# Performance work log

Measured on AMD Instinct MI355X. Metric: run time of the kernel, lower is better.

## Reference

```python
import jax, jax.numpy as jnp
import numpy as np

# Mamba2 defaults: d_model=256, d_state=64, d_conv=4, expand=2, headdim=64, ngroups=1
D_MODEL = 256
NB = 2            # num_blocks
D_STATE = 64
D_CONV = 4
D_INNER = 2 * D_MODEL          # 512
HEADDIM = 64
NHEADS = D_INNER // HEADDIM    # 8
CONV_DIM = D_INNER + 2 * D_STATE           # 640
D_IN_PROJ = 2 * D_INNER + 2 * D_STATE + NHEADS  # 1160
EPS = 1e-5


def setup_inputs() -> dict:
    key = jax.random.key(0)
    ks = jax.random.split(key, 10)
    x = jax.random.normal(ks[0], (8, 32, 32, D_MODEL), dtype=jnp.float32)
    in_proj_w = jax.random.normal(ks[1], (NB, D_IN_PROJ, D_MODEL), dtype=jnp.float32) * 0.02
    conv_w = jax.random.normal(ks[2], (NB, CONV_DIM, 1, D_CONV), dtype=jnp.float32) * 0.2
    conv_b = jax.random.normal(ks[3], (NB, CONV_DIM), dtype=jnp.float32) * 0.02
    dt_bias = jax.random.normal(ks[4], (NB, NHEADS), dtype=jnp.float32) * 0.5
    # A_log = log(A), A ~ U[1,16) as in mamba2 init
    A_log = jnp.log(jax.random.uniform(ks[5], (NB, NHEADS), minval=1.0, maxval=16.0, dtype=jnp.float32))
    D = jax.random.normal(ks[6], (NB, NHEADS), dtype=jnp.float32) * 0.1 + 1.0
    norm_w = jnp.ones((NB, D_INNER), dtype=jnp.float32)
    out_proj_w = jax.random.normal(ks[7], (NB, D_MODEL, D_INNER), dtype=jnp.float32) * 0.02
    return {"x": x, "in_proj_w": in_proj_w, "conv_w": conv_w, "conv_b": conv_b,
            "dt_bias": dt_bias, "A_log": A_log, "D": D, "norm_w": norm_w,
            "out_proj_w": out_proj_w}


def _mamba2_block(h, wi, cw, cb, dtb, a_log, d_skip, nw, wo):
    B, L, _ = h.shape
    zxbcdt = jnp.einsum('blc,pc->blp', h, wi)                 # (B,L,1160)
    z = zxbcdt[..., :D_INNER]                                 # (B,L,512)
    xBC = zxbcdt[..., D_INNER:D_INNER + CONV_DIM]             # (B,L,640)
    dt = jax.nn.softplus(zxbcdt[..., -NHEADS:] + dtb)         # (B,L,8)

    # causal depthwise conv1d, kernel 4, left pad 3
    xBC = jax.lax.conv_general_dilated(
        xBC.swapaxes(1, 2), cw, window_strides=(1,), padding=[(D_CONV - 1, 0)],
        dimension_numbers=('NCH', 'OIH', 'NCH'), feature_group_count=CONV_DIM)
    xBC = jax.nn.silu((xBC + cb[None, :, None]).swapaxes(1, 2))  # (B,L,640)

    xs = xBC[..., :D_INNER].reshape(B, L, NHEADS, HEADDIM)    # (B,L,h,p)
    Bm = xBC[..., D_INNER:D_INNER + D_STATE]                  # (B,L,s) ngroups=1
    Cm = xBC[..., D_INNER + D_STATE:]                         # (B,L,s)

    A = -jnp.exp(a_log)                                       # (h,)
    dA = jnp.exp(dt * A)                                      # (B,L,h)

    def step(s, inp):
        dA_t, dt_t, x_t, B_t, C_t = inp  # (B,h),(B,h),(B,h,p),(B,s),(B,s)
        s = s * dA_t[:, :, None, None] + (dt_t[:, :, None] * x_t)[..., None] * B_t[:, None, None, :]
        y = jnp.einsum('bhps,bs->bhp', s, C_t)
        return s, y

    s0 = jnp.zeros((B, NHEADS, HEADDIM, D_STATE), dtype=h.dtype)
    _, ys = jax.lax.scan(step, s0, (dA.swapaxes(0, 1), dt.swapaxes(0, 1),
                                    xs.swapaxes(0, 1), Bm.swapaxes(0, 1), Cm.swapaxes(0, 1)))
    y = ys.swapaxes(0, 1) + d_skip[:, None] * xs              # (B,L,h,p)
    y = y.reshape(B, L, D_INNER) * jax.nn.silu(z)             # gate
    y = y * jax.lax.rsqrt(jnp.mean(y * y, axis=-1, keepdims=True) + EPS) * nw  # gated RMSNorm
    return jnp.einsum('bld,cd->blc', y, wo)


def reference(x, in_proj_w, conv_w, conv_b, dt_bias, A_log, D, norm_w, out_proj_w):
    B, H, W, C = x.shape
    h = x.reshape(B, H * W, C)
    for i in range(NB):  # stacked blocks; Dropout is identity at inference
        h = _mamba2_block(h, in_proj_w[i], conv_w[i], conv_b[i], dt_bias[i],
                          A_log[i], D[i], norm_w[i], out_proj_w[i])
    return h.reshape(B, H, W, C)
```

## Files before the change

### kernel.cpp

```cpp
#include <hip/hip_runtime.h>
#include <hip/hip_bf16.h>
#include <math.h>

#define D_MODEL   256
#define D_STATE   64
#define D_CONV    4
#define D_INNER   512
#define HEADDIM   64
#define NHEADS    8
#define CONV_DIM  640
#define D_IN_PROJ 1160
#define ZXP       1280
#define SEQLEN    1024
#define BATCH     8
#define NROWS     8192
#define EPS       1e-5f
#define CHUNK     64
#define NCHUNK    (SEQLEN / CHUNK)

typedef __attribute__((ext_vector_type(8))) short bf16x8;
typedef __attribute__((ext_vector_type(4))) short s16x4;
typedef __attribute__((ext_vector_type(8))) unsigned short u16x8;
typedef __attribute__((ext_vector_type(4))) unsigned short u16x4;
typedef __attribute__((ext_vector_type(4))) float f32x4;
typedef unsigned int u32;
typedef unsigned short u16;

__device__ __forceinline__ void cp16(const short* g, short* l) {
    __builtin_amdgcn_global_load_lds((const __attribute__((address_space(1))) u32*)g,
                                     (__attribute__((address_space(3))) u32*)l, 16, 0, 0);
}
__device__ __forceinline__ u16 bfc(float f) {
    union { __hip_bfloat16 h; u16 u; } cv;
    cv.h = __float2bfloat16(f);
    return cv.u;
}
__device__ __forceinline__ float bf2f(u16 u) {
    union { u32 v; float f; } cv;
    cv.v = ((u32)u) << 16;
    return cv.f;
}
__device__ __forceinline__ float silu_f(float a) {
    return a * __builtin_amdgcn_rcpf(1.f + __expf(-a));
}
__device__ __forceinline__ void store_out(float* p, float v) { *p = v; }
__device__ __forceinline__ void store_out(__hip_bfloat16* p, float v) { *p = __float2bfloat16(v); }

__device__ __forceinline__ int swz(int row, int col) {
    return row * 64 + (((col & 56) ^ ((row & 7) << 3)) | (col & 7));
}
__device__ __forceinline__ bf16x8 ldfrag(const short* base, int row, int oct) {
    return *(const bf16x8*)&base[row * 64 + ((oct * 8) ^ ((row & 7) * 8))];
}
__device__ __forceinline__ void wr2u(short* base, int row, int col2, u16 a, u16 b) {
    int idx = row * 64 + (((col2 & 56) ^ ((row & 7) << 3)) | (col2 & 6));
    *(u32*)&base[idx] = (u32)a | ((u32)b << 16);
}

template <typename OUT, bool WITH_DT, bool SCALE>
__global__ __launch_bounds__(256) void gemm_mfma(const short* __restrict__ A,
                                                 const short* __restrict__ W,
                                                 OUT* __restrict__ C,
                                                 float* __restrict__ dtout,
                                                 const float* __restrict__ sc,
                                                 int N, int K, int lda) {
    __shared__ short As[128 * 32];
    __shared__ short Ws[128 * 32];
    const int tid  = threadIdx.x;
    const int m0   = blockIdx.y * 128;
    const int n0   = blockIdx.x * 128;
    const int wave = tid >> 6;
    const int lane = tid & 63;
    const int wm   = (wave & 1) * 64;
    const int wn   = (wave >> 1) * 64;
    const int lm   = lane & 15;
    const int lq   = lane >> 4;

    const int sr = tid >> 2;
    const int sk = (tid & 3) * 8;
    const short* ga = A + (size_t)(m0 + sr) * lda + sk;
    const short* gw = W + (size_t)(n0 + sr) * K + sk;
    short* la = &As[tid * 8];
    short* lw = &Ws[tid * 8];
    const size_t ga2 = (size_t)64 * lda;
    const size_t gw2 = (size_t)64 * K;

    f32x4 acc[4][4] = {};

    for (int k0 = 0; k0 < K; k0 += 32) {
        cp16(ga,       la);
        cp16(ga + ga2, la + 64 * 32);
        cp16(gw,       lw);
        cp16(gw + gw2, lw + 64 * 32);
        ga += 32; gw += 32;
        __syncthreads();
        bf16x8 af[4], bfr[4];
        #pragma unroll
        for (int i = 0; i < 4; i++) {
            af[i]  = *(const bf16x8*)&As[(wm + i * 16 + lm) * 32 + lq * 8];
            bfr[i] = *(const bf16x8*)&Ws[(wn + i * 16 + lm) * 32 + lq * 8];
        }
        #pragma unroll
        for (int i = 0; i < 4; i++)
            #pragma unroll
            for (int j = 0; j < 4; j++)
                acc[i][j] = __builtin_amdgcn_mfma_f32_16x16x32_bf16(af[i], bfr[j], acc[i][j], 0, 0, 0);
        __syncthreads();
    }
    #pragma unroll
    for (int i = 0; i < 4; i++)
        #pragma unroll
        for (int r = 0; r < 4; r++) {
            int m = m0 + wm + i * 16 + lq * 4 + r;
            float scl = SCALE ? rsqrtf(sc[m] * (1.f / (float)D_INNER) + EPS) : 1.f;
            #pragma unroll
            for (int j = 0; j < 4; j++) {
                int n = n0 + wn + j * 16 + lm;
                float v = acc[i][j][r];
                store_out(&C[(size_t)m * N + n], v * scl);
                if (WITH_DT) {
                    if (n >= D_IN_PROJ - NHEADS && n < D_IN_PROJ)
                        dtout[(size_t)m * NHEADS + (n - (D_IN_PROJ - NHEADS))] = v;
                }
            }
        }
}

#define NX_C  (NROWS * D_MODEL)
#define NWI_C (2 * ZXP * D_MODEL)
#define NWO_C (2 * D_MODEL * D_INNER)
__global__ __launch_bounds__(256) void cast_all_kernel(
    const float* __restrict__ x, const float* __restrict__ wi,
    const float* __restrict__ wo,
    u16* __restrict__ xb, u16* __restrict__ wib, u16* __restrict__ wob)
{
    int idx = blockIdx.x * 256 + threadIdx.x;
    if (idx < NX_C) { xb[idx] = bfc(x[idx]); return; }
    idx -= NX_C;
    if (idx < NWI_C) {
        int k = idx & 255;
        int rb = idx >> 8;
        int r = rb % ZXP;
        int blk = rb / ZXP;
        float v = (r < D_IN_PROJ)
            ? wi[(size_t)blk * D_IN_PROJ * D_MODEL + (size_t)r * D_MODEL + k] : 0.f;
        wib[idx] = bfc(v);
        return;
    }
    idx -= NWI_C;
    wob[idx] = bfc(wo[idx]);
}

__global__ __launch_bounds__(256) void conv_silu_kernel(const u16* __restrict__ zx,
                                                        const float* __restrict__ cw,
                                                        const float* __restrict__ cb,
                                                        u16* __restrict__ out,
                                                        u16* __restrict__ Cb) {
    int idx = blockIdx.x * 256 + threadIdx.x;
    int c4  = (idx % 160) * 4;
    int r4  = (idx / 160) * 4;
    int l4  = r4 & (SEQLEN - 1);
    float wt[4][4];
    #pragma unroll
    for (int k = 0; k < 4; k++)
        *(float4*)&wt[k][0] = *(const float4*)&cw[(c4 + k) * 4];
    float4 cbv = *(const float4*)&cb[c4];
    float cbk[4] = {cbv.x, cbv.y, cbv.z, cbv.w};

    const u16* base = zx + (size_t)r4 * ZXP + D_INNER + c4;
    u16x4 hrow[7];
    #pragma unroll
    for (int k = 0; k < 3; k++) {
        if (l4 != 0) hrow[k] = *(const u16x4*)&base[(k - 3) * ZXP];
        else { hrow[k][0] = 0; hrow[k][1] = 0; hrow[k][2] = 0; hrow[k][3] = 0; }
    }
    #pragma unroll
    for (int k = 3; k < 7; k++)
        hrow[k] = *(const u16x4*)&base[(k - 3) * ZXP];

    const bool isC = (c4 >= D_INNER + D_STATE);
    #pragma unroll
    for (int rr = 0; rr < 4; rr++) {
        u16x4 o;
        #pragma unroll
        for (int k = 0; k < 4; k++) {
            float acc = cbk[k];
            #pragma unroll
            for (int tap = 0; tap < 4; tap++)
                acc = fmaf(bf2f(hrow[rr + tap][k]), wt[k][tap], acc);
            o[k] = bfc(silu_f(acc));
        }
        *(u16x4*)&out[(size_t)(r4 + rr) * CONV_DIM + c4] = o;
        if (isC)
            *(u16x4*)&Cb[(size_t)(r4 + rr) * 64 + (c4 - (D_INNER + D_STATE))] = o;
    }
}

__global__ __launch_bounds__(256) void ssd_intra_kernel(
    const u16* __restrict__ xc, const float* __restrict__ dtbuf,
    const float* __restrict__ dt_bias, const float* __restrict__ A_log,
    const float* __restrict__ Dp,
    u16* __restrict__ ys, u16* __restrict__ Schunk,
    float* __restrict__ adec, float* __restrict__ ssum)
{
    const int h   = blockIdx.x & 7;
    const int c   = (blockIdx.x >> 3) & 15;
    const int b   = blockIdx.x >> 7;
    const int tid = threadIdx.x;
    const int row0 = b * SEQLEN + c * CHUNK;

    if (tid < 8) ssum[blockIdx.x * 8 + tid] = 0.f;

    __shared__ short Xt[64 * 64];
    __shared__ short Bn[64 * 64];
    __shared__ short Cn[64 * 64];
    __shared__ short BTw[64 * 64];
    __shared__ float cums[64], dts_s[64], ws_s[64];

    if (tid < 64) {
        const float A = -__expf(A_log[h] * 1.44269504089f);
        float raw = dtbuf[(size_t)(row0 + tid) * NHEADS + h] + dt_bias[h];
        float dtv = (raw > 20.f) ? raw : log1pf(__expf(raw));
        float v = dtv * A;
        #pragma unroll
        for (int off = 1; off < 64; off <<= 1) {
            float o = __shfl_up(v, off, 64);
            if (tid >= off) v += o;
        }
        float tot = __shfl(v, 63, 64);
        cums[tid]  = v;
        dts_s[tid] = dtv;
        ws_s[tid]  = __expf(tot - v) * dtv;
        adec[(size_t)(b * NHEADS + h) * SEQLEN + c * CHUNK + tid] = __expf(v);
    }
    __syncthreads();

    {
        const int t2 = (tid >> 3) * 2;
        const int c8 = (tid & 7) * 8;
        const u16* r0 = xc + (size_t)(row0 + t2) * CONV_DIM;
        const u16* r1 = r0 + CONV_DIM;
        u16x8 xv0 = *(const u16x8*)&r0[h * HEADDIM + c8];
        u16x8 xv1 = *(const u16x8*)&r1[h * HEADDIM + c8];
        u16x8 bv0 = *(const u16x8*)&r0[D_INNER + c8];
        u16x8 bv1 = *(const u16x8*)&r1[D_INNER + c8];
        u16x8 cv0 = *(const u16x8*)&r0[D_INNER + D_STATE + c8];
        u16x8 cv1 = *(const u16x8*)&r1[D_INNER + D_STATE + c8];
        *(u16x8*)&Bn[swz(t2,     c8)] = bv0;
        *(u16x8*)&Bn[swz(t2 + 1, c8)] = bv1;
        *(u16x8*)&Cn[swz(t2,     c8)] = cv0;
        *(u16x8*)&Cn[swz(t2 + 1, c8)] = cv1;
        float w0 = ws_s[t2], w1 = ws_s[t2 + 1];
        #pragma unroll
        for (int k = 0; k < 8; k++) {
            wr2u(Xt,  c8 + k, t2, xv0[k], xv1[k]);
            wr2u(BTw, c8 + k, t2, bfc(bf2f(bv0[k]) * w0), bfc(bf2f(bv1[k]) * w1));
        }
    }
    __syncthreads();

    const int lane = tid & 63, w = tid >> 6;
    const int lm = lane & 15, lq = lane >> 4;
    const int tau0 = 16 * w + lq * 4;

    bf16x8 aG0 = ldfrag(Bn, 16 * w + lm, lq);
    bf16x8 aG1 = ldfrag(Bn, 16 * w + lm, 4 + lq);
    f32x4 g[4] = {};
    #pragma unroll
    for (int j = 0; j < 4; j++) {
        g[j] = __builtin_amdgcn_mfma_f32_16x16x32_bf16(aG0, ldfrag(Cn, 16 * j + lm, lq),     g[j], 0, 0, 0);
        g[j] = __builtin_amdgcn_mfma_f32_16x16x32_bf16(aG1, ldfrag(Cn, 16 * j + lm, 4 + lq), g[j], 0, 0, 0);
    }
    float ctau[4], dtau[4];
    *(float4*)&ctau[0] = *(const float4*)&cums[tau0];
    *(float4*)&dtau[0] = *(const float4*)&dts_s[tau0];
    s16x4 mp[4];
    #pragma unroll
    for (int j = 0; j < 4; j++) {
        int t = 16 * j + lm;
        float ct = cums[t];
        #pragma unroll
        for (int r = 0; r < 4; r++) {
            int tau = tau0 + r;
            float m = (t >= tau) ? g[j][r] * __expf(ct - ctau[r]) * dtau[r] : 0.f;
            mp[j][r] = (short)bfc(m);
        }
    }
    __syncthreads();
    #pragma unroll
    for (int j = 0; j < 4; j++)
        *(s16x4*)&Cn[swz(16 * j + lm, tau0)] = mp[j];
    __syncthreads();

    bf16x8 aY0 = ldfrag(Cn,  16 * w + lm, lq);
    bf16x8 aY1 = ldfrag(Cn,  16 * w + lm, 4 + lq);
    bf16x8 aS0 = ldfrag(BTw, 16 * w + lm, lq);
    bf16x8 aS1 = ldfrag(BTw, 16 * w + lm, 4 + lq);
    f32x4 yv[4] = {}, sv[4] = {};
    #pragma unroll
    for (int j = 0; j < 4; j++) {
        bf16x8 xf0 = ldfrag(Xt, 16 * j + lm, lq);
        bf16x8 xf1 = ldfrag(Xt, 16 * j + lm, 4 + lq);
        yv[j] = __builtin_amdgcn_mfma_f32_16x16x32_bf16(aY0, xf0, yv[j], 0, 0, 0);
        yv[j] = __builtin_amdgcn_mfma_f32_16x16x32_bf16(aY1, xf1, yv[j], 0, 0, 0);
        sv[j] = __builtin_amdgcn_mfma_f32_16x16x32_bf16(aS0, xf0, sv[j], 0, 0, 0);
        sv[j] = __builtin_amdgcn_mfma_f32_16x16x32_bf16(aS1, xf1, sv[j], 0, 0, 0);
    }
    const float Dh = Dp[h];
    const int mrow = 16 * w + lq * 4;
    #pragma unroll
    for (int j = 0; j < 4; j++)
        #pragma unroll
        for (int r = 0; r < 4; r++) {
            float xv = bf2f((u16)Xt[swz(16 * j + lm, mrow + r)]);
            ys[(size_t)(row0 + mrow + r) * D_INNER + h * HEADDIM + 16 * j + lm]
                = bfc(yv[j][r] + Dh * xv);
        }
    u16* sb = Schunk + (size_t)((b * NCHUNK + c) * NHEADS + h) * 4096;
    #pragma unroll
    for (int j = 0; j < 4; j++)
        #pragma unroll
        for (int r = 0; r < 4; r++)
            sb[(mrow + r) * 64 + 16 * j + lm] = bfc(sv[j][r]);
}

__global__ __launch_bounds__(256) void ssd_state_scan_kernel(
    u16* __restrict__ Schunk, const float* __restrict__ adec)
{
    const int q  = blockIdx.x & 3;
    const int bh = blockIdx.x >> 2;
    const int b  = bh >> 3, h = bh & 7;
    const int base = q * 1024 + threadIdx.x * 4;

    u16x4 v[NCHUNK];
    float atot[NCHUNK];
    #pragma unroll
    for (int c = 0; c < NCHUNK; c++) {
        v[c] = *(const u16x4*)&Schunk[(size_t)((b * NCHUNK + c) * NHEADS + h) * 4096 + base];
        atot[c] = adec[(size_t)bh * SEQLEN + c * CHUNK + 63];
    }
    float run[4] = {0.f, 0.f, 0.f, 0.f};
    #pragma unroll
    for (int c = 0; c < NCHUNK; c++) {
        u16x4 pv;
        #pragma unroll
        for (int k = 0; k < 4; k++) pv[k] = bfc(run[k]);
        *(u16x4*)&Schunk[(size_t)((b * NCHUNK + c) * NHEADS + h) * 4096 + base] = pv;
        #pragma unroll
        for (int k = 0; k < 4; k++)
            run[k] = fmaf(atot[c], run[k], bf2f(v[c][k]));
    }
}

__global__ __launch_bounds__(128) void ssd_finish_kernel(
    const u16* __restrict__ Cb, const u16* __restrict__ zx,
    const u16* __restrict__ Schunk, const float* __restrict__ adec,
    const float* __restrict__ nw,
    u16* __restrict__ ys, float* __restrict__ ssum)
{
    const int hp   = blockIdx.x & 3;
    const int half = (blockIdx.x >> 2) & 1;
    const int c    = (blockIdx.x >> 3) & 15;
    const int b    = blockIdx.x >> 7;
    const int h0   = hp * 2;
    const int tid  = threadIdx.x;
    const int row0 = b * SEQLEN + c * CHUNK + half * 32;

    __shared__ short Ct[32 * 64];
    __shared__ short STs[64 * 64];
    __shared__ float a_s[64];
    __shared__ float nw_s[128];

    {
        int t2 = (tid >> 3) * 2, n8 = (tid & 7) * 8;
        const u16* r0 = Cb + (size_t)(row0 + t2) * 64;
        u16x8 v0 = *(const u16x8*)&r0[n8];
        u16x8 v1 = *(const u16x8*)&r0[64 + n8];
        *(u16x8*)&Ct[swz(t2,     n8)] = v0;
        *(u16x8*)&Ct[swz(t2 + 1, n8)] = v1;
        if (tid < 16) {
            int hh = tid >> 3, t4 = (tid & 7) * 4;
            *(float4*)&a_s[hh * 32 + t4] = *(const float4*)
                &adec[(size_t)(b * NHEADS + h0 + hh) * SEQLEN + c * CHUNK + half * 32 + t4];
        }
        nw_s[tid] = nw[h0 * 64 + tid];
    }

    const int lane = tid & 63, w = tid >> 6;
    const int lm = lane & 15, lq = lane >> 4;
    const int trow = 16 * w + lq * 4;

    bf16x8 aC0, aC1;
    float ss[4] = {0.f, 0.f, 0.f, 0.f};

    for (int hi = 0; hi < 2; hi++) {
        const int h = h0 + hi;
        {
            const u16* sb = Schunk + (size_t)((b * NCHUNK + c) * NHEADS + h) * 4096;
            int n4 = (tid >> 3) * 4, p8 = (tid & 7) * 8;
            u16x8 s0 = *(const u16x8*)&sb[(n4 + 0) * 64 + p8];
            u16x8 s1 = *(const u16x8*)&sb[(n4 + 1) * 64 + p8];
            u16x8 s2 = *(const u16x8*)&sb[(n4 + 2) * 64 + p8];
            u16x8 s3 = *(const u16x8*)&sb[(n4 + 3) * 64 + p8];
            #pragma unroll
            for (int k = 0; k < 8; k++) {
                wr2u(STs, p8 + k, n4,     s0[k], s1[k]);
                wr2u(STs, p8 + k, n4 + 2, s2[k], s3[k]);
            }
        }
        __syncthreads();
        if (hi == 0) {
            aC0 = ldfrag(Ct, 16 * w + lm, lq);
            aC1 = ldfrag(Ct, 16 * w + lm, 4 + lq);
        }
        f32x4 U[4] = {};
        #pragma unroll
        for (int j = 0; j < 4; j++) {
            U[j] = __builtin_amdgcn_mfma_f32_16x16x32_bf16(aC0, ldfrag(STs, 16 * j + lm, lq),     U[j], 0, 0, 0);
            U[j] = __builtin_amdgcn_mfma_f32_16x16x32_bf16(aC1, ldfrag(STs, 16 * j + lm, 4 + lq), U[j], 0, 0, 0);
        }
        #pragma unroll
        for (int j = 0; j < 4; j++) {
            int col = h * 64 + 16 * j + lm;
            float nwv = nw_s[hi * 64 + 16 * j + lm];
            #pragma unroll
            for (int r = 0; r < 4; r++) {
                int row = trow + r;
                size_t grow = (size_t)(row0 + row);
                float a = a_s[hi * 32 + row];
                float u = U[j][r] * a + bf2f(ys[grow * D_INNER + col]);
                float zv = bf2f(zx[grow * ZXP + col]);
                float v = u * silu_f(zv);
                ss[r] = fmaf(v, v, ss[r]);
                ys[grow * D_INNER + col] = bfc(v * nwv);
            }
        }
        __syncthreads();
    }
    #pragma unroll
    for (int r = 0; r < 4; r++) {
        float s = ss[r];
        s += __shfl_xor(s, 1, 64); s += __shfl_xor(s, 2, 64);
        s += __shfl_xor(s, 4, 64); s += __shfl_xor(s, 8, 64);
        if (lm == 0)
            atomicAdd(&ssum[row0 + trow + r], s);
    }
}

extern "C" void kernel_launch(void* const* d_in, const int* in_sizes, int n_in,
                              void* d_out, int out_size, void* d_ws, size_t ws_size,
                              hipStream_t stream) {
    const float* x          = (const float*)d_in[0];
    const float* in_proj_w  = (const float*)d_in[1];
    const float* conv_w     = (const float*)d_in[2];
    const float* conv_b     = (const float*)d_in[3];
    const float* dt_bias    = (const float*)d_in[4];
    const float* A_log      = (const float*)d_in[5];
    const float* Dp         = (const float*)d_in[6];
    const float* norm_w     = (const float*)d_in[7];
    const float* out_proj_w = (const float*)d_in[8];
    float* out = (float*)d_out;

    u16*   buf_zx = (u16*)d_ws;
    u16*   buf_xc = buf_zx + (size_t)NROWS * ZXP;
    u16*   buf_cb = buf_xc + (size_t)NROWS * CONV_DIM;
    u16*   buf_ys = buf_cb + (size_t)NROWS * 64;
    u16*   buf_S  = buf_ys + (size_t)NROWS * D_INNER;
    u16*   buf_hb = buf_S  + (size_t)BATCH * NCHUNK * NHEADS * 4096;
    u16*   buf_wi = buf_hb + (size_t)NROWS * D_MODEL;
    u16*   buf_wo = buf_wi + (size_t)2 * ZXP * D_MODEL;
    float* buf_dt = (float*)(buf_wo + (size_t)2 * D_MODEL * D_INNER);
    float* buf_a  = buf_dt + (size_t)NROWS * NHEADS;
    float* buf_sc = buf_a  + (size_t)BATCH * NHEADS * SEQLEN;

    cast_all_kernel<<<(NX_C + NWI_C + NWO_C) / 256, 256, 0, stream>>>(
        x, in_proj_w, out_proj_w, buf_hb, buf_wi, buf_wo);

    for (int i = 0; i < 2; i++) {
        gemm_mfma<__hip_bfloat16, true, false><<<dim3(ZXP / 128, NROWS / 128), 256, 0, stream>>>(
            (const short*)buf_hb, (const short*)(buf_wi + (size_t)i * ZXP * D_MODEL),
            (__hip_bfloat16*)buf_zx, buf_dt, nullptr, ZXP, D_MODEL, D_MODEL);

        conv_silu_kernel<<<(NROWS / 4) * 160 / 256, 256, 0, stream>>>(
            buf_zx, conv_w + (size_t)i * CONV_DIM * D_CONV,
            conv_b + (size_t)i * CONV_DIM, buf_xc, buf_cb);

        ssd_intra_kernel<<<BATCH * NCHUNK * NHEADS, 256, 0, stream>>>(
            buf_xc, buf_dt, dt_bias + i * NHEADS, A_log + i * NHEADS,
            Dp + i * NHEADS,
            buf_ys, buf_S, buf_a, buf_sc);

        ssd_state_scan_kernel<<<BATCH * NHEADS * 4, 256, 0, stream>>>(buf_S, buf_a);

        ssd_finish_kernel<<<BATCH * NCHUNK * 2 * 4, 128, 0, stream>>>(
            buf_cb, buf_zx, buf_S, buf_a,
            norm_w + (size_t)i * D_INNER, buf_ys, buf_sc);

        if (i == 0) {
            gemm_mfma<__hip_bfloat16, false, true><<<dim3(D_MODEL / 128, NROWS / 128), 256, 0, stream>>>(
                (const short*)buf_ys, (const short*)buf_wo,
                (__hip_bfloat16*)buf_hb, nullptr, buf_sc, D_MODEL, D_INNER, D_INNER);
        } else {
            gemm_mfma<float, false, true><<<dim3(D_MODEL / 128, NROWS / 128), 256, 0, stream>>>(
                (const short*)buf_ys, (const short*)(buf_wo + (size_t)D_MODEL * D_INNER),
                out, nullptr, buf_sc, D_MODEL, D_INNER, D_INNER);
        }
    }
}
```

Measured before the change: 201.3 us.

## Fuse SSD finish, gated RMSNorm and out-projection GEMM into one kernel

Merges the SSD finish kernel (inter-chunk state contribution, gating, norm-weight multiply) with the out_proj GEMM. The gated y tile for a 32-row slice now stays in LDS, the RMS scale is reduced in-block, and the weights are streamed through LDS for an MFMA GEMM. This removes the ys round trip through global memory, the ssum atomics and zeroing, and one launch per block. In exchange only 256 blocks of 512 threads run, with heavy LDS use, and each block re-reads the whole out_proj weight matrix.

Result: faster. 181.9 us (-9.6%).

```diff
diff --git a/kernel.cpp b/kernel.cpp
--- a/kernel.cpp
+++ b/kernel.cpp
@@ -57,12 +57,11 @@
     *(u32*)&base[idx] = (u32)a | ((u32)b << 16);
 }
 
-template <typename OUT, bool WITH_DT, bool SCALE>
+template <typename OUT, bool WITH_DT>
 __global__ __launch_bounds__(256) void gemm_mfma(const short* __restrict__ A,
                                                  const short* __restrict__ W,
                                                  OUT* __restrict__ C,
                                                  float* __restrict__ dtout,
-                                                 const float* __restrict__ sc,
                                                  int N, int K, int lda) {
     __shared__ short As[128 * 32];
     __shared__ short Ws[128 * 32];
@@ -112,12 +111,11 @@
         #pragma unroll
         for (int r = 0; r < 4; r++) {
             int m = m0 + wm + i * 16 + lq * 4 + r;
-            float scl = SCALE ? rsqrtf(sc[m] * (1.f / (float)D_INNER) + EPS) : 1.f;
             #pragma unroll
             for (int j = 0; j < 4; j++) {
                 int n = n0 + wn + j * 16 + lm;
                 float v = acc[i][j][r];
-                store_out(&C[(size_t)m * N + n], v * scl);
+                store_out(&C[(size_t)m * N + n], v);
                 if (WITH_DT) {
                     if (n >= D_IN_PROJ - NHEADS && n < D_IN_PROJ)
                         dtout[(size_t)m * NHEADS + (n - (D_IN_PROJ - NHEADS))] = v;
@@ -201,15 +199,13 @@
     const float* __restrict__ dt_bias, const float* __restrict__ A_log,
     const float* __restrict__ Dp,
     u16* __restrict__ ys, u16* __restrict__ Schunk,
-    float* __restrict__ adec, float* __restrict__ ssum)
+    float* __restrict__ adec)
 {
     const int h   = blockIdx.x & 7;
     const int c   = (blockIdx.x >> 3) & 15;
     const int b   = blockIdx.x >> 7;
     const int tid = threadIdx.x;
     const int row0 = b * SEQLEN + c * CHUNK;
-
-    if (tid < 8) ssum[blockIdx.x * 8 + tid] = 0.f;
 
     __shared__ short Xt[64 * 64];
     __shared__ short Bn[64 * 64];
@@ -352,98 +348,133 @@
     }
 }
 
-__global__ __launch_bounds__(128) void ssd_finish_kernel(
+template <typename OUT>
+__global__ __launch_bounds__(512) void ssd_finish_proj_kernel(
     const u16* __restrict__ Cb, const u16* __restrict__ zx,
-    const u16* __restrict__ Schunk, const float* __restrict__ adec,
-    const float* __restrict__ nw,
-    u16* __restrict__ ys, float* __restrict__ ssum)
+    const u16* __restrict__ ysin, const u16* __restrict__ Schunk,
+    const float* __restrict__ adec, const float* __restrict__ nw,
+    const u16* __restrict__ wo, OUT* __restrict__ Cout)
 {
-    const int hp   = blockIdx.x & 3;
-    const int half = (blockIdx.x >> 2) & 1;
-    const int c    = (blockIdx.x >> 3) & 15;
-    const int b    = blockIdx.x >> 7;
-    const int h0   = hp * 2;
+    const int half = blockIdx.x & 1;
+    const int c    = (blockIdx.x >> 1) & 15;
+    const int b    = blockIdx.x >> 5;
     const int tid  = threadIdx.x;
     const int row0 = b * SEQLEN + c * CHUNK + half * 32;
 
-    __shared__ short Ct[32 * 64];
-    __shared__ short STs[64 * 64];
-    __shared__ float a_s[64];
-    __shared__ float nw_s[128];
-
-    {
-        int t2 = (tid >> 3) * 2, n8 = (tid & 7) * 8;
-        const u16* r0 = Cb + (size_t)(row0 + t2) * 64;
-        u16x8 v0 = *(const u16x8*)&r0[n8];
-        u16x8 v1 = *(const u16x8*)&r0[64 + n8];
-        *(u16x8*)&Ct[swz(t2,     n8)] = v0;
-        *(u16x8*)&Ct[swz(t2 + 1, n8)] = v1;
-        if (tid < 16) {
-            int hh = tid >> 3, t4 = (tid & 7) * 4;
-            *(float4*)&a_s[hh * 32 + t4] = *(const float4*)
-                &adec[(size_t)(b * NHEADS + h0 + hh) * SEQLEN + c * CHUNK + half * 32 + t4];
-        }
-        nw_s[tid] = nw[h0 * 64 + tid];
-    }
+    __shared__ short y_lds[32 * 512];
+    __shared__ short reg2[256 * 64];
+    __shared__ float a_s[256];
+    __shared__ float nw_s[512];
+    __shared__ float ps[128];
+    __shared__ float scl[32];
+
+    short* Ct  = reg2;
+    short* STs = reg2 + 32 * 64;
+    short* Ws  = reg2;
 
     const int lane = tid & 63, w = tid >> 6;
     const int lm = lane & 15, lq = lane >> 4;
-    const int trow = 16 * w + lq * 4;
-
-    bf16x8 aC0, aC1;
-    float ss[4] = {0.f, 0.f, 0.f, 0.f};
-
-    for (int hi = 0; hi < 2; hi++) {
-        const int h = h0 + hi;
+    const int rf  = w & 1;
+    const int cf4 = w >> 1;
+
+    nw_s[tid] = nw[tid];
+    if (tid < 256) {
+        int t2 = tid >> 3, n8 = (tid & 7) * 8;
+        *(u16x8*)&Ct[swz(t2, n8)] = *(const u16x8*)&Cb[(size_t)(row0 + t2) * 64 + n8];
+        a_s[tid] = adec[(size_t)(b * NHEADS + (tid >> 5)) * SEQLEN + c * CHUNK + half * 32 + (tid & 31)];
+        const u16* sb = Schunk + (size_t)((b * NCHUNK + c) * NHEADS) * 4096;
+        int n2 = (tid >> 3) * 2, p8 = (tid & 7) * 8;
+        u16x8 s0 = *(const u16x8*)&sb[(size_t)n2 * 64 + p8];
+        u16x8 s1 = *(const u16x8*)&sb[(size_t)(n2 + 1) * 64 + p8];
+        #pragma unroll
+        for (int k = 0; k < 8; k++)
+            wr2u(STs, p8 + k, n2, s0[k], s1[k]);
+    }
+    __syncthreads();
+
+    bf16x8 aC0 = ldfrag(Ct, 16 * rf + lm, lq);
+    bf16x8 aC1 = ldfrag(Ct, 16 * rf + lm, 4 + lq);
+    float ssloc[4] = {0.f, 0.f, 0.f, 0.f};
+
+    for (int h = 0; h < 8; h++) {
+        const int n = cf4 * 16 + lm;
+        f32x4 U = {};
+        U = __builtin_amdgcn_mfma_f32_16x16x32_bf16(aC0, ldfrag(STs, n, lq),     U, 0, 0, 0);
+        U = __builtin_amdgcn_mfma_f32_16x16x32_bf16(aC1, ldfrag(STs, n, 4 + lq), U, 0, 0, 0);
+        __syncthreads();
+        if (h < 7 && tid < 256) {
+            const u16* sb = Schunk + (size_t)((b * NCHUNK + c) * NHEADS + h + 1) * 4096;
+            int n2 = (tid >> 3) * 2, p8 = (tid & 7) * 8;
+            u16x8 s0 = *(const u16x8*)&sb[(size_t)n2 * 64 + p8];
+            u16x8 s1 = *(const u16x8*)&sb[(size_t)(n2 + 1) * 64 + p8];
+            #pragma unroll
+            for (int k = 0; k < 8; k++)
+                wr2u(STs, p8 + k, n2, s0[k], s1[k]);
+        }
         {
-            const u16* sb = Schunk + (size_t)((b * NCHUNK + c) * NHEADS + h) * 4096;
-            int n4 = (tid >> 3) * 4, p8 = (tid & 7) * 8;
-            u16x8 s0 = *(const u16x8*)&sb[(n4 + 0) * 64 + p8];
-            u16x8 s1 = *(const u16x8*)&sb[(n4 + 1) * 64 + p8];
-            u16x8 s2 = *(const u16x8*)&sb[(n4 + 2) * 64 + p8];
-            u16x8 s3 = *(const u16x8*)&sb[(n4 + 3) * 64 + p8];
-            #pragma unroll
-            for (int k = 0; k < 8; k++) {
-                wr2u(STs, p8 + k, n4,     s0[k], s1[k]);
-                wr2u(STs, p8 + k, n4 + 2, s2[k], s3[k]);
-            }
-        }
-        __syncthreads();
-        if (hi == 0) {
-            aC0 = ldfrag(Ct, 16 * w + lm, lq);
-            aC1 = ldfrag(Ct, 16 * w + lm, 4 + lq);
-        }
-        f32x4 U[4] = {};
-        #pragma unroll
-        for (int j = 0; j < 4; j++) {
-            U[j] = __builtin_amdgcn_mfma_f32_16x16x32_bf16(aC0, ldfrag(STs, 16 * j + lm, lq),     U[j], 0, 0, 0);
-            U[j] = __builtin_amdgcn_mfma_f32_16x16x32_bf16(aC1, ldfrag(STs, 16 * j + lm, 4 + lq), U[j], 0, 0, 0);
-        }
-        #pragma unroll
-        for (int j = 0; j < 4; j++) {
-            int col = h * 64 + 16 * j + lm;
-            float nwv = nw_s[hi * 64 + 16 * j + lm];
+            const int col = h * 64 + cf4 * 16 + lm;
+            const float nwv = nw_s[col];
             #pragma unroll
             for (int r = 0; r < 4; r++) {
-                int row = trow + r;
+                int row = 16 * rf + lq * 4 + r;
                 size_t grow = (size_t)(row0 + row);
-                float a = a_s[hi * 32 + row];
-                float u = U[j][r] * a + bf2f(ys[grow * D_INNER + col]);
+                float u = U[r] * a_s[h * 32 + row] + bf2f(ysin[grow * D_INNER + col]);
                 float zv = bf2f(zx[grow * ZXP + col]);
                 float v = u * silu_f(zv);
-                ss[r] = fmaf(v, v, ss[r]);
-                ys[grow * D_INNER + col] = bfc(v * nwv);
+                ssloc[r] = fmaf(v, v, ssloc[r]);
+                y_lds[row * 512 + ((((col >> 3) ^ (row & 7)) << 3) | (col & 7))] = (short)bfc(v * nwv);
             }
         }
         __syncthreads();
     }
+
     #pragma unroll
     for (int r = 0; r < 4; r++) {
-        float s = ss[r];
+        float s = ssloc[r];
         s += __shfl_xor(s, 1, 64); s += __shfl_xor(s, 2, 64);
         s += __shfl_xor(s, 4, 64); s += __shfl_xor(s, 8, 64);
-        if (lm == 0)
-            atomicAdd(&ssum[row0 + trow + r], s);
+        if (lm == 0) ps[cf4 * 32 + 16 * rf + lq * 4 + r] = s;
+    }
+    __syncthreads();
+    if (tid < 32)
+        scl[tid] = rsqrtf((ps[tid] + ps[32 + tid] + ps[64 + tid] + ps[96 + tid])
+                          * (1.f / (float)D_INNER) + EPS);
+    __syncthreads();
+
+    f32x4 acc[4] = {};
+    const int arow = 16 * rf + lm;
+    for (int kk = 0; kk < 8; kk++) {
+        {
+            int rr = tid >> 3;
+            int oc = tid & 7;
+            #pragma unroll
+            for (int q = 0; q < 4; q++) {
+                int row = rr + q * 64;
+                const u16* src = wo + (size_t)row * 512 + kk * 64 + ((oc ^ (row & 7)) * 8);
+                cp16((const short*)src, &Ws[q * 4096 + tid * 8]);
+            }
+        }
+        __syncthreads();
+        bf16x8 aY0 = *(const bf16x8*)&y_lds[arow * 512 + ((kk * 8) | (lq       ^ (arow & 7))) * 8];
+        bf16x8 aY1 = *(const bf16x8*)&y_lds[arow * 512 + ((kk * 8) | ((4 + lq) ^ (arow & 7))) * 8];
+        #pragma unroll
+        for (int j = 0; j < 4; j++) {
+            int n = cf4 * 64 + j * 16 + lm;
+            acc[j] = __builtin_amdgcn_mfma_f32_16x16x32_bf16(aY0, ldfrag(Ws, n, lq),     acc[j], 0, 0, 0);
+            acc[j] = __builtin_amdgcn_mfma_f32_16x16x32_bf16(aY1, ldfrag(Ws, n, 4 + lq), acc[j], 0, 0, 0);
+        }
+        __syncthreads();
+    }
+    const int mrow = 16 * rf + lq * 4;
+    #pragma unroll
+    for (int r = 0; r < 4; r++) {
+        float scale = scl[mrow + r];
+        size_t m = (size_t)(row0 + mrow + r);
+        #pragma unroll
+        for (int j = 0; j < 4; j++) {
+            int n = cf4 * 64 + j * 16 + lm;
+            store_out(&Cout[m * D_MODEL + n], acc[j][r] * scale);
+        }
     }
 }
 
@@ -471,15 +502,14 @@
     u16*   buf_wo = buf_wi + (size_t)2 * ZXP * D_MODEL;
     float* buf_dt = (float*)(buf_wo + (size_t)2 * D_MODEL * D_INNER);
     float* buf_a  = buf_dt + (size_t)NROWS * NHEADS;
-    float* buf_sc = buf_a  + (size_t)BATCH * NHEADS * SEQLEN;
 
     cast_all_kernel<<<(NX_C + NWI_C + NWO_C) / 256, 256, 0, stream>>>(
         x, in_proj_w, out_proj_w, buf_hb, buf_wi, buf_wo);
 
     for (int i = 0; i < 2; i++) {
-        gemm_mfma<__hip_bfloat16, true, false><<<dim3(ZXP / 128, NROWS / 128), 256, 0, stream>>>(
+        gemm_mfma<__hip_bfloat16, true><<<dim3(ZXP / 128, NROWS / 128), 256, 0, stream>>>(
             (const short*)buf_hb, (const short*)(buf_wi + (size_t)i * ZXP * D_MODEL),
-            (__hip_bfloat16*)buf_zx, buf_dt, nullptr, ZXP, D_MODEL, D_MODEL);
+            (__hip_bfloat16*)buf_zx, buf_dt, ZXP, D_MODEL, D_MODEL);
 
         conv_silu_kernel<<<(NROWS / 4) * 160 / 256, 256, 0, stream>>>(
             buf_zx, conv_w + (size_t)i * CONV_DIM * D_CONV,
@@ -487,23 +517,18 @@
 
         ssd_intra_kernel<<<BATCH * NCHUNK * NHEADS, 256, 0, stream>>>(
             buf_xc, buf_dt, dt_bias + i * NHEADS, A_log + i * NHEADS,
-            Dp + i * NHEADS,
-            buf_ys, buf_S, buf_a, buf_sc);
+            Dp + i * NHEADS, buf_ys, buf_S, buf_a);
 
         ssd_state_scan_kernel<<<BATCH * NHEADS * 4, 256, 0, stream>>>(buf_S, buf_a);
 
-        ssd_finish_kernel<<<BATCH * NCHUNK * 2 * 4, 128, 0, stream>>>(
-            buf_cb, buf_zx, buf_S, buf_a,
-            norm_w + (size_t)i * D_INNER, buf_ys, buf_sc);
-
         if (i == 0) {
-            gemm_mfma<__hip_bfloat16, false, true><<<dim3(D_MODEL / 128, NROWS / 128), 256, 0, stream>>>(
-                (const short*)buf_ys, (const short*)buf_wo,
-                (__hip_bfloat16*)buf_hb, nullptr, buf_sc, D_MODEL, D_INNER, D_INNER);
+            ssd_finish_proj_kernel<__hip_bfloat16><<<BATCH * NCHUNK * 2, 512, 0, stream>>>(
+                buf_cb, buf_zx, buf_ys, buf_S, buf_a,
+                norm_w, (const u16*)buf_wo, (__hip_bfloat16*)buf_hb);
         } else {
-            gemm_mfma<float, false, true><<<dim3(D_MODEL / 128, NROWS / 128), 256, 0, stream>>>(
-                (const short*)buf_ys, (const short*)(buf_wo + (size_t)D_MODEL * D_INNER),
-                out, nullptr, buf_sc, D_MODEL, D_INNER, D_INNER);
-        }
-    }
-}
+            ssd_finish_proj_kernel<float><<<BATCH * NCHUNK * 2, 512, 0, stream>>>(
+                buf_cb, buf_zx, buf_ys, buf_S, buf_a,
+                norm_w + D_INNER, (const u16*)(buf_wo + (size_t)D_MODEL * D_INNER), out);
+        }
+    }
+}
```
